# Kernel optimization log

Measured on AMD Instinct MI355X. Metric: run time of the kernel, lower is better.

Reference implementation:

```python
import jax, jax.numpy as jnp
import numpy as np

B, T, H, W = 2, 16, 16, 16
C_IN, C_ORIG, N_RES, KC, VC = 256, 3, 4, 16, 128
C_ATT = C_IN + C_ORIG          # 259, used for 1/sqrt(c) scale
C_PE = C_ATT + 3               # 262, conv input channels after pos-enc concat
NEG = jnp.float32(-1e30)


def setup_inputs() -> dict:
    key = jax.random.key(0)
    ks = jax.random.split(key, 12)
    f32 = jnp.float32

    def wt(k, shape, fan_in):
        return (jax.random.normal(k, shape, dtype=f32) / np.float32(np.sqrt(fan_in)))

    return {
        "x": jax.random.normal(ks[0], (B, C_IN, T, H, W), dtype=f32),
        "original_input": jax.random.normal(ks[1], (B, C_ORIG, T, H, W), dtype=f32),
        # residual blocks (stacked over N_RES): kernel-2 conv3d, padding 1
        "rb_w1": wt(ks[2], (N_RES, C_IN, C_IN, 2, 2, 2), C_IN * 8),
        "rb_b1": jnp.zeros((N_RES, C_IN), f32),
        "rb_w2": wt(ks[3], (N_RES, 2 * C_IN, C_IN, 2, 2, 2), C_IN * 8),
        "rb_b2": jnp.zeros((N_RES, 2 * C_IN), f32),
        # attention q/k/v 1x1 conv3d == per-pixel linear on 262 channels
        "q_w": wt(ks[4], (KC, C_PE), C_PE), "q_b": jnp.zeros((KC,), f32),
        "k_w": wt(ks[5], (KC, C_PE), C_PE), "k_b": jnp.zeros((KC,), f32),
        "v_w": wt(ks[6], (VC, C_PE), C_PE), "v_b": jnp.zeros((VC,), f32),
        # attention_conv (1x1), res_conv (1x1), out_conv (1x1)
        "attn_w": wt(ks[7], (C_IN, VC), VC), "attn_b": jnp.zeros((C_IN,), f32),
        "resc_w": wt(ks[8], (C_IN, C_IN), C_IN), "resc_b": jnp.zeros((C_IN,), f32),
        "out_w": wt(ks[9], (C_IN, C_IN), C_IN), "out_b": jnp.zeros((C_IN,), f32),
    }


def _conv3d(x, w, b, pad):
    y = jax.lax.conv_general_dilated(
        x, w, window_strides=(1, 1, 1), padding=[(pad, pad)] * 3,
        dimension_numbers=("NCDHW", "OIDHW", "NCDHW"))
    return y + b[None, :, None, None, None]


def _c1(x, w, b):  # 1x1x1 conv
    return jnp.einsum("bcthw,oc->bothw", x, w) + b[None, :, None, None, None]


def _pos_enc(b, t, h, w):
    zt = (-0.5 + jnp.arange(t, dtype=jnp.float32) / t)[None, None, :, None, None]
    zh = (-0.5 + jnp.arange(h, dtype=jnp.float32) / h)[None, None, None, :, None]
    zw = (-0.5 + jnp.arange(w, dtype=jnp.float32) / w)[None, None, None, None, :]
    shp = (b, 1, t, h, w)
    return jnp.concatenate([jnp.broadcast_to(zt, shp),
                            jnp.broadcast_to(zh, shp),
                            jnp.broadcast_to(zw, shp)], axis=1)


def _forward(x, original_input, rb_w1, rb_b1, rb_w2, rb_b2,
             q_w, q_b, k_w, k_b, v_w, v_b,
             attn_w, attn_b, resc_w, resc_b, out_w, out_b):
    b, _, t, h, w = x.shape
    elu = jax.nn.elu

    # --- residual blocks (attention=True variant: k=2 convs, pad=1, crop) ---
    res = x
    for i in range(N_RES):
        o = elu(_conv3d(elu(res), rb_w1[i], rb_b1[i], 1))[:, :, :t, :h, :w]
        o = _conv3d(o, rb_w2[i], rb_b2[i], 1)[:, :, :t, :h, :w]
        c2 = o.shape[1] // 2
        res = res + o[:, :c2] * jax.nn.sigmoid(o[:, c2:])  # gated (identity act)

    # --- attention block on concat(res, original_input) + pos-enc ---
    xa = jnp.concatenate([res, original_input], axis=1)          # (b,259,t,h,w)
    xa = jnp.concatenate([xa, _pos_enc(b, t, h, w)], axis=1)     # (b,262,t,h,w)
    seq = t * h * w
    xf = xa.reshape(b, C_PE, seq).transpose(0, 2, 1)             # (b,seq,262)
    q = xf @ q_w.T + q_b
    k = xf @ k_w.T + k_b
    v = xf @ v_w.T + v_b                                         # (b,seq,VC)

    scores = jnp.einsum("bqc,bkc->bqk", q, k) / np.float32(np.sqrt(C_ATT))
    mask = jnp.tril(jnp.ones((seq, seq), dtype=bool), k=-1)      # mask_center=True
    p = jax.nn.softmax(jnp.where(mask, scores, NEG), axis=-1)
    p = jnp.where(mask, p, 0.0)                                  # row 0 -> zeros
    att = jnp.einsum("bqk,bkc->bqc", p, v)                       # (b,seq,VC)
    att = att.transpose(0, 2, 1).reshape(b, VC, t, h, w)

    att = elu(_c1(elu(att), attn_w, attn_b))
    res = elu(_c1(elu(res), resc_w, resc_b))
    return elu(_c1(elu(res + att), out_w, out_b))


def reference(x, original_input, rb_w1, rb_b1, rb_w2, rb_b2,
              q_w, q_b, k_w, k_b, v_w, v_b,
              attn_w, attn_b, resc_w, resc_b, out_w, out_b):
    return _forward(x, original_input, rb_w1, rb_b1, rb_w2, rb_b2,
                    q_w, q_b, k_w, k_b, v_w, v_b,
                    attn_w, attn_b, resc_w, resc_b, out_w, out_b)
```

## Files before the change

### kernel.cpp

```cpp
#include <hip/hip_runtime.h>
#include <math.h>

#define SEQ 4096
#define CIN 256
#define PROWS 4913
#define PT 289
#define LROW 40
#define NROWS 170

typedef __attribute__((ext_vector_type(8))) short bf16x8;
typedef __attribute__((ext_vector_type(4))) float f32x4;

__device__ __forceinline__ float elu_f(float x) {
    return x > 0.0f ? x : (expf(x) - 1.0f);
}
__device__ __forceinline__ unsigned short f2b(float f) {
    unsigned int u = __float_as_uint(f);
    return (unsigned short)((u + 0x7FFFu + ((u >> 16) & 1u)) >> 16);
}

__global__ __launch_bounds__(256) void zero2_kernel(
    uint4* __restrict__ p1, uint4* __restrict__ p2, int n)
{
    int i = blockIdx.x * 256 + threadIdx.x;
    if (i < n) {
        p1[i] = (uint4){0, 0, 0, 0};
        p2[i] = (uint4){0, 0, 0, 0};
    }
}

__global__ __launch_bounds__(256) void prep_t(
    const float* __restrict__ x, unsigned short* __restrict__ elub)
{
    const int b = blockIdx.x >> 5;
    const int s0 = (blockIdx.x & 31) << 7;
    const int cg = blockIdx.y;
    const int tid = threadIdx.x;
    const int s = s0 + (tid & 127);
    const int c0 = cg * 32 + (tid >> 7) * 16;
    const int tt = s >> 8, hh = (s >> 4) & 15, ww = s & 15;
    const size_t prow = (size_t)b * PROWS + (tt + 1) * PT + (hh + 1) * 17 + (ww + 1);
    unsigned short ev[16];
#pragma unroll
    for (int cc = 0; cc < 16; ++cc) {
        float v = x[(((size_t)(b * 256 + c0 + cc)) << 12) + s];
        ev[cc] = f2b(elu_f(v));
    }
    unsigned short* ep = &elub[prow * 256 + c0];
    *(ushort4*)(ep)      = *(ushort4*)&ev[0];
    *(ushort4*)(ep + 4)  = *(ushort4*)&ev[4];
    *(ushort4*)(ep + 8)  = *(ushort4*)&ev[8];
    *(ushort4*)(ep + 12) = *(ushort4*)&ev[12];
}

__global__ __launch_bounds__(256) void wcvt_kernel(
    const float* __restrict__ w1, const float* __restrict__ w2,
    unsigned short* __restrict__ w1t, unsigned short* __restrict__ w2t)
{
    int idx = blockIdx.x * 256 + threadIdx.x;
    if (idx < 2097152) {
        int layer = idx >> 19;
        int rem = idx & 0x7FFFF;
        int frag = rem >> 9;
        int l = (rem >> 3) & 63;
        int e = rem & 7;
        int ks = frag >> 4, mt = frag & 15;
        int tap = ks >> 3, kc = ks & 7;
        int co = mt * 16 + (l & 15);
        int ci = kc * 32 + (l >> 4) * 8 + e;
        w1t[idx] = f2b(w1[(((size_t)(layer * 256 + co)) * 256 + ci) * 8 + tap]);
    }
    if (idx < 4194304) {
        int layer = idx >> 20;
        int rem = idx & 0xFFFFF;
        int frag = rem >> 9;
        int l = (rem >> 3) & 63;
        int e = rem & 7;
        int ks = frag >> 5, mt = frag & 31;
        int tap = ks >> 3, kc = ks & 7;
        int rp = mt * 16 + (l & 15);
        int grp = rp >> 5, sub = rp & 31;
        int co = (sub < 16) ? (grp * 16 + sub) : (256 + grp * 16 + (sub - 16));
        int ci = kc * 32 + (l >> 4) * 8 + e;
        w2t[idx] = f2b(w2[(((size_t)(layer * 512 + co)) * 256 + ci) * 8 + tap]);
    }
}

__global__ __launch_bounds__(256) void conv1_mfma(
    const unsigned short* __restrict__ inP,
    const unsigned short* __restrict__ wfrag,
    const float* __restrict__ bias,
    unsigned short* __restrict__ outP)
{
    __shared__ unsigned short sX[NROWS * LROW];

    const int bx = blockIdx.x;
    const int b = bx >> 6, ptile = bx & 63;
    const int t = ptile >> 2, h0 = (ptile & 3) << 2;
    const int mt0 = blockIdx.y << 2;
    const int tid = threadIdx.x;
    const int lane = tid & 63, wv = tid >> 6;
    const int lr = lane & 15, lg = lane >> 4;

    const unsigned short* inB = inP + (size_t)b * PROWS * 256;

    f32x4 acc[4];
#pragma unroll
    for (int mi = 0; mi < 4; ++mi) acc[mi] = (f32x4){0.f, 0.f, 0.f, 0.f};

    for (int kc = 0; kc < 8; ++kc) {
        const int ci0 = kc << 5;
        __syncthreads();
#pragma unroll
        for (int rnd = 0; rnd < 3; ++rnd) {
            int task = tid + (rnd << 8);
            int row = task >> 2, q = task & 3;
            if (row < NROWS) {
                int dt = row / 85, rem = row - dt * 85;
                int dh = rem / 17, dw = rem - dh * 17;
                int prow = (t + dt) * PT + (h0 + dh) * 17 + dw;
                *(bf16x8*)&sX[row * LROW + (q << 3)] =
                    *(const bf16x8*)(inB + (size_t)prow * 256 + ci0 + (q << 3));
            }
        }
        __syncthreads();
#pragma unroll
        for (int tap = 0; tap < 8; ++tap) {
            const unsigned short* wp = wfrag +
                ((size_t)((((tap << 3) + kc) << 4) + mt0) << 9) + (lane << 3);
            bf16x8 a0 = *(const bf16x8*)(wp);
            bf16x8 a1 = *(const bf16x8*)(wp + 512);
            bf16x8 a2 = *(const bf16x8*)(wp + 1024);
            bf16x8 a3 = *(const bf16x8*)(wp + 1536);
            const int rb = (tap >> 2) * 85 + (wv + ((tap >> 1) & 1)) * 17 + (tap & 1);
            bf16x8 xb = *(const bf16x8*)&sX[(rb + lr) * LROW + (lg << 3)];
            acc[0] = __builtin_amdgcn_mfma_f32_16x16x32_bf16(a0, xb, acc[0], 0, 0, 0);
            acc[1] = __builtin_amdgcn_mfma_f32_16x16x32_bf16(a1, xb, acc[1], 0, 0, 0);
            acc[2] = __builtin_amdgcn_mfma_f32_16x16x32_bf16(a2, xb, acc[2], 0, 0, 0);
            acc[3] = __builtin_amdgcn_mfma_f32_16x16x32_bf16(a3, xb, acc[3], 0, 0, 0);
        }
    }
    const size_t orow = (size_t)b * PROWS + (t + 1) * PT + (h0 + wv + 1) * 17 + (lr + 1);
#pragma unroll
    for (int mi = 0; mi < 4; ++mi) {
        const int cob = ((mt0 + mi) << 4) + (lg << 2);
        unsigned short v4[4];
#pragma unroll
        for (int r = 0; r < 4; ++r)
            v4[r] = f2b(elu_f(acc[mi][r] + bias[cob + r]));
        *(ushort4*)&outP[orow * 256 + cob] = *(ushort4*)v4;
    }
}

__global__ __launch_bounds__(256) void conv2_mfma(
    const unsigned short* __restrict__ inP,
    const unsigned short* __restrict__ wfrag,
    const float* __restrict__ bias,
    float* __restrict__ resf,
    unsigned short* __restrict__ elub)
{
    __shared__ unsigned short sX[NROWS * LROW];

    const int bx = blockIdx.x;
    const int b = bx >> 6, ptile = bx & 63;
    const int t = ptile >> 2, h0 = (ptile & 3) << 2;
    const int mt0 = blockIdx.y << 2;
    const int tid = threadIdx.x;
    const int lane = tid & 63, wv = tid >> 6;
    const int lr = lane & 15, lg = lane >> 4;

    const unsigned short* inB = inP + (size_t)b * PROWS * 256;

    f32x4 acc[4];
#pragma unroll
    for (int mi = 0; mi < 4; ++mi) acc[mi] = (f32x4){0.f, 0.f, 0.f, 0.f};

    for (int kc = 0; kc < 8; ++kc) {
        const int ci0 = kc << 5;
        __syncthreads();
#pragma unroll
        for (int rnd = 0; rnd < 3; ++rnd) {
            int task = tid + (rnd << 8);
            int row = task >> 2, q = task & 3;
            if (row < NROWS) {
                int dt = row / 85, rem = row - dt * 85;
                int dh = rem / 17, dw = rem - dh * 17;
                int prow = (t + dt) * PT + (h0 + dh) * 17 + dw;
                *(bf16x8*)&sX[row * LROW + (q << 3)] =
                    *(const bf16x8*)(inB + (size_t)prow * 256 + ci0 + (q << 3));
            }
        }
        __syncthreads();
#pragma unroll
        for (int tap = 0; tap < 8; ++tap) {
            const unsigned short* wp = wfrag +
                ((size_t)((((tap << 3) + kc) << 5) + mt0) << 9) + (lane << 3);
            bf16x8 a0 = *(const bf16x8*)(wp);
            bf16x8 a1 = *(const bf16x8*)(wp + 512);
            bf16x8 a2 = *(const bf16x8*)(wp + 1024);
            bf16x8 a3 = *(const bf16x8*)(wp + 1536);
            const int rb = (tap >> 2) * 85 + (wv + ((tap >> 1) & 1)) * 17 + (tap & 1);
            bf16x8 xb = *(const bf16x8*)&sX[(rb + lr) * LROW + (lg << 3)];
            acc[0] = __builtin_amdgcn_mfma_f32_16x16x32_bf16(a0, xb, acc[0], 0, 0, 0);
            acc[1] = __builtin_amdgcn_mfma_f32_16x16x32_bf16(a1, xb, acc[1], 0, 0, 0);
            acc[2] = __builtin_amdgcn_mfma_f32_16x16x32_bf16(a2, xb, acc[2], 0, 0, 0);
            acc[3] = __builtin_amdgcn_mfma_f32_16x16x32_bf16(a3, xb, acc[3], 0, 0, 0);
        }
    }
    const int s = (t << 8) + ((h0 + wv) << 4) + lr;
    const size_t prow = (size_t)b * PROWS + (t + 1) * PT + (h0 + wv + 1) * 17 + (lr + 1);
#pragma unroll
    for (int p = 0; p < 2; ++p) {
        const int chb = (((mt0 >> 1) + p) << 4) + (lg << 2);
        unsigned short e4[4];
#pragma unroll
        for (int r = 0; r < 4; ++r) {
            const int ch = chb + r;
            float av = acc[2 * p][r] + bias[ch];
            float gv = acc[2 * p + 1][r] + bias[ch + 256];
            float add = av / (1.0f + expf(-gv));
            size_t ridx = (((size_t)(b * 256 + ch)) << 12) + s;
            float rn = resf[ridx] + add;
            resf[ridx] = rn;
            e4[r] = f2b(elu_f(rn));
        }
        *(ushort4*)&elub[prow * 256 + chb] = *(ushort4*)e4;
    }
}

__global__ __launch_bounds__(256) void pack_kernel(
    const float* __restrict__ res, const float* __restrict__ orig,
    unsigned short* __restrict__ xq)
{
    const int b = blockIdx.x >> 5;
    const int s0 = (blockIdx.x & 31) << 7;
    const int cg = blockIdx.y;
    const int tid = threadIdx.x;
    const int s = s0 + (tid & 127);
    const int c0 = cg * 32 + (tid >> 7) * 16;

    unsigned short xv[16];
    if (cg < 8) {
#pragma unroll
        for (int cc = 0; cc < 16; ++cc) {
            int c = c0 + cc;
            float v = res[(size_t)((b * 256 + c) << 12) + s];
            xv[cc] = f2b(v);
        }
    } else if (cg == 8) {
#pragma unroll
        for (int cc = 0; cc < 16; ++cc) {
            int c = c0 + cc;
            float v;
            if (c < 259)      v = orig[(size_t)((b * 3 + (c - 256)) << 12) + s];
            else if (c == 259) v = -0.5f + (float)(s >> 8) * 0.0625f;
            else if (c == 260) v = -0.5f + (float)((s >> 4) & 15) * 0.0625f;
            else if (c == 261) v = -0.5f + (float)(s & 15) * 0.0625f;
            else               v = 0.0f;
            xv[cc] = f2b(v);
        }
    } else {
#pragma unroll
        for (int cc = 0; cc < 16; ++cc) xv[cc] = 0;
    }
    unsigned short* xp = &xq[((size_t)(b << 12) + s) * 320 + c0];
    *(ushort4*)(xp)      = *(ushort4*)&xv[0];
    *(ushort4*)(xp + 4)  = *(ushort4*)&xv[4];
    *(ushort4*)(xp + 8)  = *(ushort4*)&xv[8];
    *(ushort4*)(xp + 12) = *(ushort4*)&xv[12];
}

__global__ __launch_bounds__(256) void wcvt2_kernel(
    const float* __restrict__ qw, const float* __restrict__ kw,
    const float* __restrict__ vw, const float* __restrict__ aw,
    const float* __restrict__ rw, const float* __restrict__ ow,
    unsigned short* __restrict__ wqkv, unsigned short* __restrict__ awb,
    unsigned short* __restrict__ rwb, unsigned short* __restrict__ owb)
{
    int idx = blockIdx.x * 256 + threadIdx.x;
    if (idx < 61440) {
        int r = idx / 320, c = idx - r * 320;
        float v = 0.0f;
        if (c < 262) {
            if (r < 16)       v = qw[r * 262 + c];
            else if (r < 32)  v = kw[(r - 16) * 262 + c];
            else if (r < 160) v = vw[(r - 32) * 262 + c];
        }
        wqkv[idx] = f2b(v);
    } else if (idx < 61440 + 32768) {
        int j = idx - 61440; awb[j] = f2b(aw[j]);
    } else if (idx < 61440 + 32768 + 65536) {
        int j = idx - 61440 - 32768; rwb[j] = f2b(rw[j]);
    } else if (idx < 61440 + 32768 + 131072) {
        int j = idx - 61440 - 98304; owb[j] = f2b(ow[j]);
    }
}

__global__ __launch_bounds__(256) void qkv_gemm(
    const unsigned short* __restrict__ Wb, const unsigned short* __restrict__ Xt,
    const float* __restrict__ qb, const float* __restrict__ kb,
    const float* __restrict__ vb,
    unsigned short* __restrict__ qbt, unsigned short* __restrict__ kbt,
    unsigned short* __restrict__ vbt)
{
    const int b = blockIdx.x >> 5;
    const int s0 = (blockIdx.x & 31) << 7;
    const int co0 = blockIdx.y << 6;
    const int lane = threadIdx.x & 63, wv = threadIdx.x >> 6;
    const int lr = lane & 15, lg = lane >> 4;

    f32x4 acc[4][2];
#pragma unroll
    for (int mi = 0; mi < 4; ++mi)
#pragma unroll
        for (int ni = 0; ni < 2; ++ni) acc[mi][ni] = (f32x4){0.f, 0.f, 0.f, 0.f};

    const unsigned short* wp = Wb + (size_t)co0 * 320 + lg * 8;
    const unsigned short* xp = Xt + ((size_t)(b << 12) + s0 + wv * 32) * 320 + lg * 8;

#pragma unroll
    for (int kc = 0; kc < 10; ++kc) {
        int ko = kc * 32;
        bf16x8 a[4], x[2];
#pragma unroll
        for (int mi = 0; mi < 4; ++mi)
            a[mi] = *(const bf16x8*)(wp + (size_t)(mi * 16 + lr) * 320 + ko);
#pragma unroll
        for (int ni = 0; ni < 2; ++ni)
            x[ni] = *(const bf16x8*)(xp + (size_t)(ni * 16 + lr) * 320 + ko);
#pragma unroll
        for (int mi = 0; mi < 4; ++mi)
#pragma unroll
            for (int ni = 0; ni < 2; ++ni)
                acc[mi][ni] = __builtin_amdgcn_mfma_f32_16x16x32_bf16(
                    a[mi], x[ni], acc[mi][ni], 0, 0, 0);
    }
#pragma unroll
    for (int mi = 0; mi < 4; ++mi)
#pragma unroll
    for (int ni = 0; ni < 2; ++ni)
#pragma unroll
    for (int r = 0; r < 4; ++r) {
        int co = co0 + mi * 16 + lg * 4 + r;
        if (co >= 160) continue;
        int s = s0 + wv * 32 + ni * 16 + lr;
        float bias = (co < 16) ? qb[co] : ((co < 32) ? kb[co - 16] : vb[co - 32]);
        float v = acc[mi][ni][r] + bias;
        if (co < 16)      qbt[((size_t)(b << 12) + s) * 16 + co] = f2b(v);
        else if (co < 32) kbt[((size_t)(b << 12) + s) * 16 + (co - 16)] = f2b(v);
        else              vbt[((size_t)((b << 7) + (co - 32)) << 12) + s] = f2b(v);
    }
}

__global__ __launch_bounds__(256) void attn_part2(
    const unsigned short* __restrict__ qbt, const unsigned short* __restrict__ kbt,
    const unsigned short* __restrict__ vbt,
    float* __restrict__ pacc, float* __restrict__ pml)
{
    const int bx = blockIdx.x;
    const int b = bx >> 8;
    const int qt = (bx >> 2) & 63;
    const int seg = bx & 3;
    const int q0 = qt << 6;
    const int nch = (qt >> 1) + 1;
    const int c_lo = seg << 3;
    if (c_lo >= nch) return;
    const int c_hi = min(c_lo + 8, nch);

    __shared__ unsigned short sK[128 * 16];
    __shared__ unsigned short sP[4][16 * 136];

    const int tid = threadIdx.x;
    const int lane = tid & 63, wv = tid >> 6;
    const int lr = lane & 15, lg = lane >> 4;
    const int qa = q0 + wv * 16 + lr;
    const float scale = 1.0f / sqrtf(259.0f);

    bf16x8 qf = (bf16x8){0, 0, 0, 0, 0, 0, 0, 0};
    if (lg < 2)
        qf = *(const bf16x8*)(qbt + ((size_t)(b << 12) + qa) * 16 + lg * 8);

    f32x4 oacc[8];
#pragma unroll
    for (int vct = 0; vct < 8; ++vct) oacc[vct] = (f32x4){0.f, 0.f, 0.f, 0.f};
    float m = -1e30f, l = 0.0f;

    unsigned short* myP = &sP[wv][0];

    for (int kc = c_lo; kc < c_hi; ++kc) {
        const int kv0 = kc << 7;
        __syncthreads();
        *(bf16x8*)&sK[(tid >> 1) * 16 + (tid & 1) * 8] =
            *(const bf16x8*)(kbt + ((size_t)(b << 12) + kv0 + (tid >> 1)) * 16 + (tid & 1) * 8);
        __syncthreads();

        f32x4 sc[8];
#pragma unroll
        for (int kvt = 0; kvt < 8; ++kvt) {
            bf16x8 af = (bf16x8){0, 0, 0, 0, 0, 0, 0, 0};
            if (lg < 2)
                af = *(const bf16x8*)&sK[(kvt * 16 + lr) * 16 + lg * 8];
            sc[kvt] = __builtin_amdgcn_mfma_f32_16x16x32_bf16(
                af, qf, (f32x4){0.f, 0.f, 0.f, 0.f}, 0, 0, 0);
        }
        float mc = -1e30f;
#pragma unroll
        for (int kvt = 0; kvt < 8; ++kvt) {
#pragma unroll
            for (int r = 0; r < 4; ++r) {
                int kv = kv0 + kvt * 16 + lg * 4 + r;
                float s = (kv < qa) ? sc[kvt][r] * scale : -1e30f;
                sc[kvt][r] = s;
                mc = fmaxf(mc, s);
            }
        }
        mc = fmaxf(mc, __shfl_xor(mc, 16, 64));
        mc = fmaxf(mc, __shfl_xor(mc, 32, 64));
        float mn = fmaxf(m, mc);
        float fac = __expf(m - mn);
        float ls = 0.0f;
#pragma unroll
        for (int kvt = 0; kvt < 8; ++kvt) {
#pragma unroll
            for (int e = 0; e < 2; ++e) {
                float s0v = sc[kvt][2 * e];
                float s1v = sc[kvt][2 * e + 1];
                float p0 = (s0v <= -1e29f) ? 0.f : __expf(s0v - mn);
                float p1 = (s1v <= -1e29f) ? 0.f : __expf(s1v - mn);
                ls += p0 + p1;
                unsigned int pk = (unsigned int)f2b(p0) | ((unsigned int)f2b(p1) << 16);
                int kv = kvt * 16 + lg * 4 + 2 * e;
                *(unsigned int*)&myP[lr * 136 + kv] = pk;
            }
        }
        ls += __shfl_xor(ls, 16, 64);
        ls += __shfl_xor(ls, 32, 64);
        l = l * fac + ls;
        m = mn;
#pragma unroll
        for (int vct = 0; vct < 8; ++vct) {
            oacc[vct][0] *= fac; oacc[vct][1] *= fac;
            oacc[vct][2] *= fac; oacc[vct][3] *= fac;
        }
#pragma unroll
        for (int ks = 0; ks < 4; ++ks) {
            bf16x8 pf = *(const bf16x8*)&myP[lr * 136 + ks * 32 + lg * 8];
#pragma unroll
            for (int vct = 0; vct < 8; ++vct) {
                bf16x8 vf = *(const bf16x8*)(vbt +
                    ((size_t)((b << 7) + vct * 16 + lr) << 12) + kv0 + ks * 32 + lg * 8);
                oacc[vct] = __builtin_amdgcn_mfma_f32_16x16x32_bf16(
                    vf, pf, oacc[vct], 0, 0, 0);
            }
        }
    }

    const int a_ = qt >> 4;
    const int slot = b * 160 + 8 * a_ * (a_ + 1) + (qt & 15) * (a_ + 1) + seg;
    float* ap = pacc + (size_t)slot * 8192;
#pragma unroll
    for (int vct = 0; vct < 8; ++vct)
        *(f32x4*)&ap[(wv * 16 + lr) * 128 + vct * 16 + lg * 4] = oacc[vct];
    if (lg == 0) {
        pml[slot * 128 + (wv * 16 + lr) * 2]     = m;
        pml[slot * 128 + (wv * 16 + lr) * 2 + 1] = l;
    }
}

__global__ __launch_bounds__(256) void attn_combine2(
    const float* __restrict__ pacc, const float* __restrict__ pml,
    unsigned short* __restrict__ attEb)
{
    const int bx = blockIdx.x;
    const int b = bx >> 7;
    const int qt = (bx >> 1) & 63;
    const int half = bx & 1;
    const int a_ = qt >> 4;
    const int nseg_alloc = a_ + 1;
    const int nch = (qt >> 1) + 1;
    const int nseg = (nch + 7) >> 3;
    const int base = b * 160 + 8 * a_ * (a_ + 1) + (qt & 15) * nseg_alloc;
    const int tid = threadIdx.x;
    const int qq = (tid >> 3) + half * 32;
    const int vg = tid & 7;

    float mi_[4], li_[4];
    float m = -1e30f;
    for (int i = 0; i < nseg; ++i) {
        mi_[i] = pml[(base + i) * 128 + qq * 2];
        li_[i] = pml[(base + i) * 128 + qq * 2 + 1];
        m = fmaxf(m, mi_[i]);
    }
    float w[4];
    float l = 0.f;
    for (int i = 0; i < nseg; ++i) {
        float wi = (mi_[i] <= -1e29f) ? 0.f : __expf(mi_[i] - m);
        w[i] = wi;
        l += wi * li_[i];
    }
    float inv = (l > 0.f) ? 1.f / l : 0.f;
    int q = (qt << 6) + qq;
#pragma unroll
    for (int v4 = 0; v4 < 4; ++v4) {
        int vc = vg * 16 + v4 * 4;
        float o0 = 0.f, o1 = 0.f, o2 = 0.f, o3 = 0.f;
        for (int i = 0; i < nseg; ++i) {
            f32x4 a = *(const f32x4*)(pacc + (size_t)(base + i) * 8192 + qq * 128 + vc);
            o0 = fmaf(w[i], a[0], o0);
            o1 = fmaf(w[i], a[1], o1);
            o2 = fmaf(w[i], a[2], o2);
            o3 = fmaf(w[i], a[3], o3);
        }
        unsigned short r0 = f2b(elu_f(o0 * inv));
        unsigned short r1 = f2b(elu_f(o1 * inv));
        unsigned short r2 = f2b(elu_f(o2 * inv));
        unsigned short r3 = f2b(elu_f(o3 * inv));
        ushort4 pk = {r0, r1, r2, r3};
        *(ushort4*)&attEb[((size_t)(b << 12) + q) * 128 + vc] = pk;
    }
}

__global__ __launch_bounds__(256) void final_ab_gemm(
    const unsigned short* __restrict__ W1b, const unsigned short* __restrict__ W2b,
    const unsigned short* __restrict__ X1, const unsigned short* __restrict__ X2,
    const float* __restrict__ b1, const float* __restrict__ b2,
    unsigned short* __restrict__ sum2b)
{
    const int b = blockIdx.x >> 5;
    const int s0 = (blockIdx.x & 31) << 7;
    const int co0 = blockIdx.y << 6;
    const int lane = threadIdx.x & 63, wv = threadIdx.x >> 6;
    const int lr = lane & 15, lg = lane >> 4;

    f32x4 acc1[4][2], acc2[4][2];
#pragma unroll
    for (int mi = 0; mi < 4; ++mi)
#pragma unroll
        for (int ni = 0; ni < 2; ++ni) {
            acc1[mi][ni] = (f32x4){0.f, 0.f, 0.f, 0.f};
            acc2[mi][ni] = (f32x4){0.f, 0.f, 0.f, 0.f};
        }

    {
        const unsigned short* wp = W1b + (size_t)co0 * 128 + lg * 8;
        const unsigned short* xp = X1 + ((size_t)(b << 12) + s0 + wv * 32) * 128 + lg * 8;
#pragma unroll
        for (int kc = 0; kc < 4; ++kc) {
            int ko = kc * 32;
            bf16x8 a[4], x[2];
#pragma unroll
            for (int mi = 0; mi < 4; ++mi)
                a[mi] = *(const bf16x8*)(wp + (size_t)(mi * 16 + lr) * 128 + ko);
#pragma unroll
            for (int ni = 0; ni < 2; ++ni)
                x[ni] = *(const bf16x8*)(xp + (size_t)(ni * 16 + lr) * 128 + ko);
#pragma unroll
            for (int mi = 0; mi < 4; ++mi)
#pragma unroll
                for (int ni = 0; ni < 2; ++ni)
                    acc1[mi][ni] = __builtin_amdgcn_mfma_f32_16x16x32_bf16(
                        a[mi], x[ni], acc1[mi][ni], 0, 0, 0);
        }
    }
    {
        const unsigned short* wp = W2b + (size_t)co0 * 256 + lg * 8;
        const unsigned short* xp2[2];
#pragma unroll
        for (int ni = 0; ni < 2; ++ni) {
            int u = (s0 >> 4) + wv * 2 + ni;
            int tt = u >> 4, hh = u & 15;
            xp2[ni] = X2 + ((size_t)b * PROWS + (tt + 1) * PT + (hh + 1) * 17 + (lr + 1)) * 256 + lg * 8;
        }
#pragma unroll
        for (int kc = 0; kc < 8; ++kc) {
            int ko = kc * 32;
            bf16x8 a[4], x[2];
#pragma unroll
            for (int mi = 0; mi < 4; ++mi)
                a[mi] = *(const bf16x8*)(wp + (size_t)(mi * 16 + lr) * 256 + ko);
#pragma unroll
            for (int ni = 0; ni < 2; ++ni)
                x[ni] = *(const bf16x8*)(xp2[ni] + ko);
#pragma unroll
            for (int mi = 0; mi < 4; ++mi)
#pragma unroll
                for (int ni = 0; ni < 2; ++ni)
                    acc2[mi][ni] = __builtin_amdgcn_mfma_f32_16x16x32_bf16(
                        a[mi], x[ni], acc2[mi][ni], 0, 0, 0);
        }
    }
#pragma unroll
    for (int mi = 0; mi < 4; ++mi)
#pragma unroll
    for (int ni = 0; ni < 2; ++ni)
#pragma unroll
    for (int r = 0; r < 4; ++r) {
        int co = co0 + mi * 16 + lg * 4 + r;
        int s = s0 + wv * 32 + ni * 16 + lr;
        float v1 = elu_f(acc1[mi][ni][r] + b1[co]);
        float v2 = elu_f(acc2[mi][ni][r] + b2[co]);
        sum2b[((size_t)(b << 12) + s) * 256 + co] = f2b(elu_f(v1 + v2));
    }
}

__global__ __launch_bounds__(256) void final_c_gemm(
    const unsigned short* __restrict__ Wb, const unsigned short* __restrict__ Xt,
    const float* __restrict__ bias, float* __restrict__ out)
{
    const int b = blockIdx.x >> 5;
    const int s0 = (blockIdx.x & 31) << 7;
    const int co0 = blockIdx.y << 6;
    const int lane = threadIdx.x & 63, wv = threadIdx.x >> 6;
    const int lr = lane & 15, lg = lane >> 4;

    f32x4 acc[4][2];
#pragma unroll
    for (int mi = 0; mi < 4; ++mi)
#pragma unroll
        for (int ni = 0; ni < 2; ++ni) acc[mi][ni] = (f32x4){0.f, 0.f, 0.f, 0.f};

    const unsigned short* wp = Wb + (size_t)co0 * 256 + lg * 8;
    const unsigned short* xp = Xt + ((size_t)(b << 12) + s0 + wv * 32) * 256 + lg * 8;
#pragma unroll
    for (int kc = 0; kc < 8; ++kc) {
        int ko = kc * 32;
        bf16x8 a[4], x[2];
#pragma unroll
        for (int mi = 0; mi < 4; ++mi)
            a[mi] = *(const bf16x8*)(wp + (size_t)(mi * 16 + lr) * 256 + ko);
#pragma unroll
        for (int ni = 0; ni < 2; ++ni)
            x[ni] = *(const bf16x8*)(xp + (size_t)(ni * 16 + lr) * 256 + ko);
#pragma unroll
        for (int mi = 0; mi < 4; ++mi)
#pragma unroll
            for (int ni = 0; ni < 2; ++ni)
                acc[mi][ni] = __builtin_amdgcn_mfma_f32_16x16x32_bf16(
                    a[mi], x[ni], acc[mi][ni], 0, 0, 0);
    }
#pragma unroll
    for (int mi = 0; mi < 4; ++mi)
#pragma unroll
    for (int ni = 0; ni < 2; ++ni)
#pragma unroll
    for (int r = 0; r < 4; ++r) {
        int co = co0 + mi * 16 + lg * 4 + r;
        int s = s0 + wv * 32 + ni * 16 + lr;
        out[((size_t)(b * 256 + co) << 12) + s] = elu_f(acc[mi][ni][r] + bias[co]);
    }
}

extern "C" void kernel_launch(void* const* d_in, const int* in_sizes, int n_in,
                              void* d_out, int out_size, void* d_ws, size_t ws_size,
                              hipStream_t stream) {
    const float* x      = (const float*)d_in[0];
    const float* orig   = (const float*)d_in[1];
    const float* rb_w1  = (const float*)d_in[2];
    const float* rb_b1  = (const float*)d_in[3];
    const float* rb_w2  = (const float*)d_in[4];
    const float* rb_b2  = (const float*)d_in[5];
    const float* q_w    = (const float*)d_in[6];
    const float* q_b    = (const float*)d_in[7];
    const float* k_w    = (const float*)d_in[8];
    const float* k_b    = (const float*)d_in[9];
    const float* v_w    = (const float*)d_in[10];
    const float* v_b    = (const float*)d_in[11];
    const float* attn_w = (const float*)d_in[12];
    const float* attn_b = (const float*)d_in[13];
    const float* resc_w = (const float*)d_in[14];
    const float* resc_b = (const float*)d_in[15];
    const float* out_w  = (const float*)d_in[16];
    const float* out_b  = (const float*)d_in[17];
    float* out = (float*)d_out;

    char* base = (char*)d_ws;
    float*          res   = (float*)(base);
    unsigned short* elubP = (unsigned short*)(base + (8u << 20));
    unsigned short* o1P   = (unsigned short*)(base + (13u << 20));
    unsigned short* w1t   = (unsigned short*)(base + (18u << 20));
    unsigned short* w2t   = (unsigned short*)(base + (22u << 20));
    unsigned short* vbt   = o1P;
    unsigned short* attEb = (unsigned short*)(base + (15u << 20));
    unsigned short* sum2b = w1t;
    unsigned short* xqkvB = w2t;
    float*          pacc  = (float*)(base + (22u << 20));
    unsigned short* qbt   = (unsigned short*)(base + (32u << 20));
    unsigned short* kbt   = (unsigned short*)(base + (32u << 20) + 262144);
    unsigned short* wqkvB = (unsigned short*)(base + (32u << 20) + 524288);
    unsigned short* attnWb= (unsigned short*)(base + (32u << 20) + 655360);
    unsigned short* rescWb= (unsigned short*)(base + (32u << 20) + 720896);
    unsigned short* outWb = (unsigned short*)(base + (32u << 20) + 851968);
    float*          pml   = (float*)(base + (32u << 20) + 983040);

    const int nz = (2 * PROWS * 256 * 2) / 16;
    zero2_kernel<<<(nz + 255) / 256, 256, 0, stream>>>(
        (uint4*)elubP, (uint4*)o1P, nz);

    hipMemcpyAsync(res, x, (size_t)2097152 * sizeof(float),
                   hipMemcpyDeviceToDevice, stream);
    prep_t<<<dim3(64, 8), 256, 0, stream>>>(x, elubP);
    wcvt_kernel<<<16384, 256, 0, stream>>>(rb_w1, rb_w2, w1t, w2t);

    for (int i = 0; i < 4; ++i) {
        conv1_mfma<<<dim3(128, 4), 256, 0, stream>>>(
            elubP, w1t + (size_t)i * 524288, rb_b1 + i * 256, o1P);
        conv2_mfma<<<dim3(128, 8), 256, 0, stream>>>(
            o1P, w2t + (size_t)i * 1048576, rb_b2 + i * 512, res, elubP);
    }

    pack_kernel<<<dim3(64, 10), 256, 0, stream>>>(res, orig, xqkvB);
    wcvt2_kernel<<<880, 256, 0, stream>>>(q_w, k_w, v_w, attn_w, resc_w, out_w,
                                          wqkvB, attnWb, rescWb, outWb);

    qkv_gemm<<<dim3(64, 3), 256, 0, stream>>>(wqkvB, xqkvB, q_b, k_b, v_b,
                                              qbt, kbt, vbt);

    attn_part2<<<512, 256, 0, stream>>>(qbt, kbt, vbt, pacc, pml);
    attn_combine2<<<256, 256, 0, stream>>>(pacc, pml, attEb);

    final_ab_gemm<<<dim3(64, 4), 256, 0, stream>>>(
        attnWb, rescWb, attEb, elubP, attn_b, resc_b, sum2b);

    final_c_gemm<<<dim3(64, 4), 256, 0, stream>>>(outWb, sum2b, out_b, out);
}
```

Baseline: 424.0 us.

## Store V in MFMA fragment order and preload all K chunks into LDS

The QKV GEMM now writes V in a pre-swizzled layout that matches the MFMA operand fragment. Each lane in attention can then load its V fragment as one contiguous 16-byte read, replacing the earlier strided rows. The attention kernel also loads every K chunk for its segment into shared memory up front, which removes two barriers per iteration. The cost is a larger LDS footprint (32KB for K), which may lower occupancy, and scattered 2-byte stores in the GEMM epilogue.

```diff
diff --git a/kernel.cpp b/kernel.cpp
--- a/kernel.cpp
+++ b/kernel.cpp
@@ -301,7 +301,7 @@
     const float* __restrict__ qb, const float* __restrict__ kb,
     const float* __restrict__ vb,
     unsigned short* __restrict__ qbt, unsigned short* __restrict__ kbt,
-    unsigned short* __restrict__ vbt)
+    unsigned short* __restrict__ vfrag)
 {
     const int b = blockIdx.x >> 5;
     const int s0 = (blockIdx.x & 31) << 7;
@@ -348,13 +348,21 @@
         float v = acc[mi][ni][r] + bias;
         if (co < 16)      qbt[((size_t)(b << 12) + s) * 16 + co] = f2b(v);
         else if (co < 32) kbt[((size_t)(b << 12) + s) * 16 + (co - 16)] = f2b(v);
-        else              vbt[((size_t)((b << 7) + (co - 32)) << 12) + s] = f2b(v);
+        else {
+            int vc = co - 32;
+            int kvb = s >> 7, kvo = s & 127;
+            int ksv = kvo >> 5;
+            int lfrag = (((kvo >> 3) & 3) << 4) + (vc & 15);
+            size_t addr = ((((size_t)(b * 128 + kvb * 4 + ksv)) * 8 + (vc >> 4)) << 9)
+                          + (lfrag << 3) + (kvo & 7);
+            vfrag[addr] = f2b(v);
+        }
     }
 }
 
 __global__ __launch_bounds__(256) void attn_part2(
     const unsigned short* __restrict__ qbt, const unsigned short* __restrict__ kbt,
-    const unsigned short* __restrict__ vbt,
+    const unsigned short* __restrict__ vfrag,
     float* __restrict__ pacc, float* __restrict__ pml)
 {
     const int bx = blockIdx.x;
@@ -367,7 +375,7 @@
     if (c_lo >= nch) return;
     const int c_hi = min(c_lo + 8, nch);
 
-    __shared__ unsigned short sK[128 * 16];
+    __shared__ unsigned short sK[8 * 128 * 16];
     __shared__ unsigned short sP[4][16 * 136];
 
     const int tid = threadIdx.x;
@@ -380,6 +388,13 @@
     if (lg < 2)
         qf = *(const bf16x8*)(qbt + ((size_t)(b << 12) + qa) * 16 + lg * 8);
 
+    for (int kc = c_lo; kc < c_hi; ++kc) {
+        *(bf16x8*)&sK[((kc - c_lo) << 11) + (tid >> 1) * 16 + (tid & 1) * 8] =
+            *(const bf16x8*)(kbt + ((size_t)(b << 12) + (kc << 7) + (tid >> 1)) * 16
+                             + (tid & 1) * 8);
+    }
+    __syncthreads();
+
     f32x4 oacc[8];
 #pragma unroll
     for (int vct = 0; vct < 8; ++vct) oacc[vct] = (f32x4){0.f, 0.f, 0.f, 0.f};
@@ -388,18 +403,15 @@
     unsigned short* myP = &sP[wv][0];
 
     for (int kc = c_lo; kc < c_hi; ++kc) {
+        const int kci = kc - c_lo;
         const int kv0 = kc << 7;
-        __syncthreads();
-        *(bf16x8*)&sK[(tid >> 1) * 16 + (tid & 1) * 8] =
-            *(const bf16x8*)(kbt + ((size_t)(b << 12) + kv0 + (tid >> 1)) * 16 + (tid & 1) * 8);
-        __syncthreads();
 
         f32x4 sc[8];
 #pragma unroll
         for (int kvt = 0; kvt < 8; ++kvt) {
             bf16x8 af = (bf16x8){0, 0, 0, 0, 0, 0, 0, 0};
             if (lg < 2)
-                af = *(const bf16x8*)&sK[(kvt * 16 + lr) * 16 + lg * 8];
+                af = *(const bf16x8*)&sK[(kci << 11) + (kvt * 16 + lr) * 16 + lg * 8];
             sc[kvt] = __builtin_amdgcn_mfma_f32_16x16x32_bf16(
                 af, qf, (f32x4){0.f, 0.f, 0.f, 0.f}, 0, 0, 0);
         }
@@ -442,13 +454,14 @@
             oacc[vct][0] *= fac; oacc[vct][1] *= fac;
             oacc[vct][2] *= fac; oacc[vct][3] *= fac;
         }
+        const unsigned short* vchunk = vfrag +
+            ((size_t)(b * 128 + (kv0 >> 5)) << 12) + (lane << 3);
 #pragma unroll
         for (int ks = 0; ks < 4; ++ks) {
             bf16x8 pf = *(const bf16x8*)&myP[lr * 136 + ks * 32 + lg * 8];
 #pragma unroll
             for (int vct = 0; vct < 8; ++vct) {
-                bf16x8 vf = *(const bf16x8*)(vbt +
-                    ((size_t)((b << 7) + vct * 16 + lr) << 12) + kv0 + ks * 32 + lg * 8);
+                bf16x8 vf = *(const bf16x8*)(vchunk + ((size_t)(ks * 8 + vct) << 9));
                 oacc[vct] = __builtin_amdgcn_mfma_f32_16x16x32_bf16(
                     vf, pf, oacc[vct], 0, 0, 0);
             }
@@ -679,7 +692,7 @@
     unsigned short* o1P   = (unsigned short*)(base + (13u << 20));
     unsigned short* w1t   = (unsigned short*)(base + (18u << 20));
     unsigned short* w2t   = (unsigned short*)(base + (22u << 20));
-    unsigned short* vbt   = o1P;
+    unsigned short* vfrag = o1P;
     unsigned short* attEb = (unsigned short*)(base + (15u << 20));
     unsigned short* sum2b = w1t;
     unsigned short* xqkvB = w2t;
@@ -713,9 +726,9 @@
                                           wqkvB, attnWb, rescWb, outWb);
 
     qkv_gemm<<<dim3(64, 3), 256, 0, stream>>>(wqkvB, xqkvB, q_b, k_b, v_b,
-                                              qbt, kbt, vbt);
-
-    attn_part2<<<512, 256, 0, stream>>>(qbt, kbt, vbt, pacc, pml);
+                                              qbt, kbt, vfrag);
+
+    attn_part2<<<512, 256, 0, stream>>>(qbt, kbt, vfrag, pacc, pml);
     attn_combine2<<<256, 256, 0, stream>>>(pacc, pml, attEb);
 
     final_ab_gemm<<<dim3(64, 4), 256, 0, stream>>>(
```

After: 429.4 us. No clear change (+1.3%).

## Pre-swizzle GEMM weights into MFMA fragment order and stage activations in LDS

Applied to the files above, without the earlier changes.

Weight conversion now writes the q/k/v, attention, residual and output 1x1 weights in MFMA fragment-major order, so each lane loads its A operand with one contiguous 16-byte read. The three small GEMM kernels also copy 128-row activation tiles into padded shared memory with coalesced loads before the MFMA reads, replacing strided per-lane global loads. In exchange each k-step adds two block barriers and drops full unrolling, and there is no double buffering, so loads and MFMAs may serialize.

```diff
diff --git a/kernel.cpp b/kernel.cpp
--- a/kernel.cpp
+++ b/kernel.cpp
@@ -7,6 +7,7 @@
 #define PT 289
 #define LROW 40
 #define NROWS 170
+#define GROW 36
 
 typedef __attribute__((ext_vector_type(8))) short bf16x8;
 typedef __attribute__((ext_vector_type(4))) float f32x4;
@@ -279,7 +280,10 @@
 {
     int idx = blockIdx.x * 256 + threadIdx.x;
     if (idx < 61440) {
-        int r = idx / 320, c = idx - r * 320;
+        int frag = idx >> 9, l = (idx >> 3) & 63, e = idx & 7;
+        int kc = frag / 12, mt = frag - kc * 12;
+        int r = mt * 16 + (l & 15);
+        int c = kc * 32 + ((l >> 4) << 3) + e;
         float v = 0.0f;
         if (c < 262) {
             if (r < 16)       v = qw[r * 262 + c];
@@ -287,26 +291,44 @@
             else if (r < 160) v = vw[(r - 32) * 262 + c];
         }
         wqkv[idx] = f2b(v);
-    } else if (idx < 61440 + 32768) {
-        int j = idx - 61440; awb[j] = f2b(aw[j]);
-    } else if (idx < 61440 + 32768 + 65536) {
-        int j = idx - 61440 - 32768; rwb[j] = f2b(rw[j]);
-    } else if (idx < 61440 + 32768 + 131072) {
-        int j = idx - 61440 - 98304; owb[j] = f2b(ow[j]);
+    } else if (idx < 94208) {
+        int j = idx - 61440;
+        int frag = j >> 9, l = (j >> 3) & 63, e = j & 7;
+        int kc = frag >> 4, mt = frag & 15;
+        int r = mt * 16 + (l & 15);
+        int c = kc * 32 + ((l >> 4) << 3) + e;
+        awb[j] = f2b(aw[r * 128 + c]);
+    } else if (idx < 159744) {
+        int j = idx - 94208;
+        int frag = j >> 9, l = (j >> 3) & 63, e = j & 7;
+        int kc = frag >> 4, mt = frag & 15;
+        int r = mt * 16 + (l & 15);
+        int c = kc * 32 + ((l >> 4) << 3) + e;
+        rwb[j] = f2b(rw[r * 256 + c]);
+    } else if (idx < 225280) {
+        int j = idx - 159744;
+        int frag = j >> 9, l = (j >> 3) & 63, e = j & 7;
+        int kc = frag >> 4, mt = frag & 15;
+        int r = mt * 16 + (l & 15);
+        int c = kc * 32 + ((l >> 4) << 3) + e;
+        owb[j] = f2b(ow[r * 256 + c]);
     }
 }
 
 __global__ __launch_bounds__(256) void qkv_gemm(
-    const unsigned short* __restrict__ Wb, const unsigned short* __restrict__ Xt,
+    const unsigned short* __restrict__ Wf, const unsigned short* __restrict__ Xt,
     const float* __restrict__ qb, const float* __restrict__ kb,
     const float* __restrict__ vb,
     unsigned short* __restrict__ qbt, unsigned short* __restrict__ kbt,
     unsigned short* __restrict__ vbt)
 {
+    __shared__ unsigned short sX[128 * GROW];
+
     const int b = blockIdx.x >> 5;
     const int s0 = (blockIdx.x & 31) << 7;
-    const int co0 = blockIdx.y << 6;
-    const int lane = threadIdx.x & 63, wv = threadIdx.x >> 6;
+    const int mt0 = blockIdx.y << 2;
+    const int tid = threadIdx.x;
+    const int lane = tid & 63, wv = tid >> 6;
     const int lr = lane & 15, lg = lane >> 4;
 
     f32x4 acc[4][2];
@@ -315,26 +337,34 @@
 #pragma unroll
         for (int ni = 0; ni < 2; ++ni) acc[mi][ni] = (f32x4){0.f, 0.f, 0.f, 0.f};
 
-    const unsigned short* wp = Wb + (size_t)co0 * 320 + lg * 8;
-    const unsigned short* xp = Xt + ((size_t)(b << 12) + s0 + wv * 32) * 320 + lg * 8;
-
-#pragma unroll
     for (int kc = 0; kc < 10; ++kc) {
-        int ko = kc * 32;
-        bf16x8 a[4], x[2];
-#pragma unroll
-        for (int mi = 0; mi < 4; ++mi)
-            a[mi] = *(const bf16x8*)(wp + (size_t)(mi * 16 + lr) * 320 + ko);
-#pragma unroll
-        for (int ni = 0; ni < 2; ++ni)
-            x[ni] = *(const bf16x8*)(xp + (size_t)(ni * 16 + lr) * 320 + ko);
-#pragma unroll
-        for (int mi = 0; mi < 4; ++mi)
-#pragma unroll
-            for (int ni = 0; ni < 2; ++ni)
-                acc[mi][ni] = __builtin_amdgcn_mfma_f32_16x16x32_bf16(
-                    a[mi], x[ni], acc[mi][ni], 0, 0, 0);
-    }
+        __syncthreads();
+#pragma unroll
+        for (int rnd = 0; rnd < 2; ++rnd) {
+            int task = tid + (rnd << 8);
+            int row = task >> 2, q = task & 3;
+            *(bf16x8*)&sX[row * GROW + (q << 3)] =
+                *(const bf16x8*)(Xt + ((size_t)(b << 12) + s0 + row) * 320
+                                 + kc * 32 + (q << 3));
+        }
+        __syncthreads();
+        const unsigned short* wp = Wf + ((size_t)(kc * 12 + mt0) << 9) + (lane << 3);
+        bf16x8 a0 = *(const bf16x8*)(wp);
+        bf16x8 a1 = *(const bf16x8*)(wp + 512);
+        bf16x8 a2 = *(const bf16x8*)(wp + 1024);
+        bf16x8 a3 = *(const bf16x8*)(wp + 1536);
+        bf16x8 x0 = *(const bf16x8*)&sX[(wv * 32 + lr) * GROW + (lg << 3)];
+        bf16x8 x1 = *(const bf16x8*)&sX[(wv * 32 + 16 + lr) * GROW + (lg << 3)];
+        acc[0][0] = __builtin_amdgcn_mfma_f32_16x16x32_bf16(a0, x0, acc[0][0], 0, 0, 0);
+        acc[0][1] = __builtin_amdgcn_mfma_f32_16x16x32_bf16(a0, x1, acc[0][1], 0, 0, 0);
+        acc[1][0] = __builtin_amdgcn_mfma_f32_16x16x32_bf16(a1, x0, acc[1][0], 0, 0, 0);
+        acc[1][1] = __builtin_amdgcn_mfma_f32_16x16x32_bf16(a1, x1, acc[1][1], 0, 0, 0);
+        acc[2][0] = __builtin_amdgcn_mfma_f32_16x16x32_bf16(a2, x0, acc[2][0], 0, 0, 0);
+        acc[2][1] = __builtin_amdgcn_mfma_f32_16x16x32_bf16(a2, x1, acc[2][1], 0, 0, 0);
+        acc[3][0] = __builtin_amdgcn_mfma_f32_16x16x32_bf16(a3, x0, acc[3][0], 0, 0, 0);
+        acc[3][1] = __builtin_amdgcn_mfma_f32_16x16x32_bf16(a3, x1, acc[3][1], 0, 0, 0);
+    }
+    const int co0 = mt0 << 4;
 #pragma unroll
     for (int mi = 0; mi < 4; ++mi)
 #pragma unroll
@@ -521,15 +551,18 @@
 }
 
 __global__ __launch_bounds__(256) void final_ab_gemm(
-    const unsigned short* __restrict__ W1b, const unsigned short* __restrict__ W2b,
+    const unsigned short* __restrict__ W1f, const unsigned short* __restrict__ W2f,
     const unsigned short* __restrict__ X1, const unsigned short* __restrict__ X2,
     const float* __restrict__ b1, const float* __restrict__ b2,
     unsigned short* __restrict__ sum2b)
 {
+    __shared__ unsigned short sX[128 * GROW];
+
     const int b = blockIdx.x >> 5;
     const int s0 = (blockIdx.x & 31) << 7;
-    const int co0 = blockIdx.y << 6;
-    const int lane = threadIdx.x & 63, wv = threadIdx.x >> 6;
+    const int mt0 = blockIdx.y << 2;
+    const int tid = threadIdx.x;
+    const int lane = tid & 63, wv = tid >> 6;
     const int lr = lane & 15, lg = lane >> 4;
 
     f32x4 acc1[4][2], acc2[4][2];
@@ -541,54 +574,63 @@
             acc2[mi][ni] = (f32x4){0.f, 0.f, 0.f, 0.f};
         }
 
-    {
-        const unsigned short* wp = W1b + (size_t)co0 * 128 + lg * 8;
-        const unsigned short* xp = X1 + ((size_t)(b << 12) + s0 + wv * 32) * 128 + lg * 8;
-#pragma unroll
-        for (int kc = 0; kc < 4; ++kc) {
-            int ko = kc * 32;
-            bf16x8 a[4], x[2];
-#pragma unroll
-            for (int mi = 0; mi < 4; ++mi)
-                a[mi] = *(const bf16x8*)(wp + (size_t)(mi * 16 + lr) * 128 + ko);
-#pragma unroll
-            for (int ni = 0; ni < 2; ++ni)
-                x[ni] = *(const bf16x8*)(xp + (size_t)(ni * 16 + lr) * 128 + ko);
-#pragma unroll
-            for (int mi = 0; mi < 4; ++mi)
-#pragma unroll
-                for (int ni = 0; ni < 2; ++ni)
-                    acc1[mi][ni] = __builtin_amdgcn_mfma_f32_16x16x32_bf16(
-                        a[mi], x[ni], acc1[mi][ni], 0, 0, 0);
-        }
-    }
-    {
-        const unsigned short* wp = W2b + (size_t)co0 * 256 + lg * 8;
-        const unsigned short* xp2[2];
-#pragma unroll
-        for (int ni = 0; ni < 2; ++ni) {
-            int u = (s0 >> 4) + wv * 2 + ni;
-            int tt = u >> 4, hh = u & 15;
-            xp2[ni] = X2 + ((size_t)b * PROWS + (tt + 1) * PT + (hh + 1) * 17 + (lr + 1)) * 256 + lg * 8;
-        }
-#pragma unroll
-        for (int kc = 0; kc < 8; ++kc) {
-            int ko = kc * 32;
-            bf16x8 a[4], x[2];
-#pragma unroll
-            for (int mi = 0; mi < 4; ++mi)
-                a[mi] = *(const bf16x8*)(wp + (size_t)(mi * 16 + lr) * 256 + ko);
-#pragma unroll
-            for (int ni = 0; ni < 2; ++ni)
-                x[ni] = *(const bf16x8*)(xp2[ni] + ko);
-#pragma unroll
-            for (int mi = 0; mi < 4; ++mi)
-#pragma unroll
-                for (int ni = 0; ni < 2; ++ni)
-                    acc2[mi][ni] = __builtin_amdgcn_mfma_f32_16x16x32_bf16(
-                        a[mi], x[ni], acc2[mi][ni], 0, 0, 0);
-        }
-    }
+    for (int kc = 0; kc < 4; ++kc) {
+        __syncthreads();
+#pragma unroll
+        for (int rnd = 0; rnd < 2; ++rnd) {
+            int task = tid + (rnd << 8);
+            int row = task >> 2, q = task & 3;
+            *(bf16x8*)&sX[row * GROW + (q << 3)] =
+                *(const bf16x8*)(X1 + ((size_t)(b << 12) + s0 + row) * 128
+                                 + kc * 32 + (q << 3));
+        }
+        __syncthreads();
+        const unsigned short* wp = W1f + ((size_t)((kc << 4) + mt0) << 9) + (lane << 3);
+        bf16x8 a0 = *(const bf16x8*)(wp);
+        bf16x8 a1 = *(const bf16x8*)(wp + 512);
+        bf16x8 a2 = *(const bf16x8*)(wp + 1024);
+        bf16x8 a3 = *(const bf16x8*)(wp + 1536);
+        bf16x8 x0 = *(const bf16x8*)&sX[(wv * 32 + lr) * GROW + (lg << 3)];
+        bf16x8 x1 = *(const bf16x8*)&sX[(wv * 32 + 16 + lr) * GROW + (lg << 3)];
+        acc1[0][0] = __builtin_amdgcn_mfma_f32_16x16x32_bf16(a0, x0, acc1[0][0], 0, 0, 0);
+        acc1[0][1] = __builtin_amdgcn_mfma_f32_16x16x32_bf16(a0, x1, acc1[0][1], 0, 0, 0);
+        acc1[1][0] = __builtin_amdgcn_mfma_f32_16x16x32_bf16(a1, x0, acc1[1][0], 0, 0, 0);
+        acc1[1][1] = __builtin_amdgcn_mfma_f32_16x16x32_bf16(a1, x1, acc1[1][1], 0, 0, 0);
+        acc1[2][0] = __builtin_amdgcn_mfma_f32_16x16x32_bf16(a2, x0, acc1[2][0], 0, 0, 0);
+        acc1[2][1] = __builtin_amdgcn_mfma_f32_16x16x32_bf16(a2, x1, acc1[2][1], 0, 0, 0);
+        acc1[3][0] = __builtin_amdgcn_mfma_f32_16x16x32_bf16(a3, x0, acc1[3][0], 0, 0, 0);
+        acc1[3][1] = __builtin_amdgcn_mfma_f32_16x16x32_bf16(a3, x1, acc1[3][1], 0, 0, 0);
+    }
+    for (int kc = 0; kc < 8; ++kc) {
+        __syncthreads();
+#pragma unroll
+        for (int rnd = 0; rnd < 2; ++rnd) {
+            int task = tid + (rnd << 8);
+            int row = task >> 2, q = task & 3;
+            int s = s0 + row;
+            int tt = s >> 8, hh = (s >> 4) & 15, ww = s & 15;
+            size_t prow = (size_t)b * PROWS + (tt + 1) * PT + (hh + 1) * 17 + (ww + 1);
+            *(bf16x8*)&sX[row * GROW + (q << 3)] =
+                *(const bf16x8*)(X2 + prow * 256 + kc * 32 + (q << 3));
+        }
+        __syncthreads();
+        const unsigned short* wp = W2f + ((size_t)((kc << 4) + mt0) << 9) + (lane << 3);
+        bf16x8 a0 = *(const bf16x8*)(wp);
+        bf16x8 a1 = *(const bf16x8*)(wp + 512);
+        bf16x8 a2 = *(const bf16x8*)(wp + 1024);
+        bf16x8 a3 = *(const bf16x8*)(wp + 1536);
+        bf16x8 x0 = *(const bf16x8*)&sX[(wv * 32 + lr) * GROW + (lg << 3)];
+        bf16x8 x1 = *(const bf16x8*)&sX[(wv * 32 + 16 + lr) * GROW + (lg << 3)];
+        acc2[0][0] = __builtin_amdgcn_mfma_f32_16x16x32_bf16(a0, x0, acc2[0][0], 0, 0, 0);
+        acc2[0][1] = __builtin_amdgcn_mfma_f32_16x16x32_bf16(a0, x1, acc2[0][1], 0, 0, 0);
+        acc2[1][0] = __builtin_amdgcn_mfma_f32_16x16x32_bf16(a1, x0, acc2[1][0], 0, 0, 0);
+        acc2[1][1] = __builtin_amdgcn_mfma_f32_16x16x32_bf16(a1, x1, acc2[1][1], 0, 0, 0);
+        acc2[2][0] = __builtin_amdgcn_mfma_f32_16x16x32_bf16(a2, x0, acc2[2][0], 0, 0, 0);
+        acc2[2][1] = __builtin_amdgcn_mfma_f32_16x16x32_bf16(a2, x1, acc2[2][1], 0, 0, 0);
+        acc2[3][0] = __builtin_amdgcn_mfma_f32_16x16x32_bf16(a3, x0, acc2[3][0], 0, 0, 0);
+        acc2[3][1] = __builtin_amdgcn_mfma_f32_16x16x32_bf16(a3, x1, acc2[3][1], 0, 0, 0);
+    }
+    const int co0 = mt0 << 4;
 #pragma unroll
     for (int mi = 0; mi < 4; ++mi)
 #pragma unroll
@@ -604,13 +646,16 @@
 }
 
 __global__ __launch_bounds__(256) void final_c_gemm(
-    const unsigned short* __restrict__ Wb, const unsigned short* __restrict__ Xt,
+    const unsigned short* __restrict__ Wf, const unsigned short* __restrict__ Xt,
     const float* __restrict__ bias, float* __restrict__ out)
 {
+    __shared__ unsigned short sX[128 * GROW];
+
     const int b = blockIdx.x >> 5;
     const int s0 = (blockIdx.x & 31) << 7;
-    const int co0 = blockIdx.y << 6;
-    const int lane = threadIdx.x & 63, wv = threadIdx.x >> 6;
+    const int mt0 = blockIdx.y << 2;
+    const int tid = threadIdx.x;
+    const int lane = tid & 63, wv = tid >> 6;
     const int lr = lane & 15, lg = lane >> 4;
 
     f32x4 acc[4][2];
@@ -619,25 +664,34 @@
 #pragma unroll
         for (int ni = 0; ni < 2; ++ni) acc[mi][ni] = (f32x4){0.f, 0.f, 0.f, 0.f};
 
-    const unsigned short* wp = Wb + (size_t)co0 * 256 + lg * 8;
-    const unsigned short* xp = Xt + ((size_t)(b << 12) + s0 + wv * 32) * 256 + lg * 8;
-#pragma unroll
     for (int kc = 0; kc < 8; ++kc) {
-        int ko = kc * 32;
-        bf16x8 a[4], x[2];
-#pragma unroll
-        for (int mi = 0; mi < 4; ++mi)
-            a[mi] = *(const bf16x8*)(wp + (size_t)(mi * 16 + lr) * 256 + ko);
-#pragma unroll
-        for (int ni = 0; ni < 2; ++ni)
-            x[ni] = *(const bf16x8*)(xp + (size_t)(ni * 16 + lr) * 256 + ko);
-#pragma unroll
-        for (int mi = 0; mi < 4; ++mi)
-#pragma unroll
-            for (int ni = 0; ni < 2; ++ni)
-                acc[mi][ni] = __builtin_amdgcn_mfma_f32_16x16x32_bf16(
-                    a[mi], x[ni], acc[mi][ni], 0, 0, 0);
-    }
+        __syncthreads();
+#pragma unroll
+        for (int rnd = 0; rnd < 2; ++rnd) {
+            int task = tid + (rnd << 8);
+            int row = task >> 2, q = task & 3;
+            *(bf16x8*)&sX[row * GROW + (q << 3)] =
+                *(const bf16x8*)(Xt + ((size_t)(b << 12) + s0 + row) * 256
+                                 + kc * 32 + (q << 3));
+        }
+        __syncthreads();
+        const unsigned short* wp = Wf + ((size_t)((kc << 4) + mt0) << 9) + (lane << 3);
+        bf16x8 a0 = *(const bf16x8*)(wp);
+        bf16x8 a1 = *(const bf16x8*)(wp + 512);
+        bf16x8 a2 = *(const bf16x8*)(wp + 1024);
+        bf16x8 a3 = *(const bf16x8*)(wp + 1536);
+        bf16x8 x0 = *(const bf16x8*)&sX[(wv * 32 + lr) * GROW + (lg << 3)];
+        bf16x8 x1 = *(const bf16x8*)&sX[(wv * 32 + 16 + lr) * GROW + (lg << 3)];
+        acc[0][0] = __builtin_amdgcn_mfma_f32_16x16x32_bf16(a0, x0, acc[0][0], 0, 0, 0);
+        acc[0][1] = __builtin_amdgcn_mfma_f32_16x16x32_bf16(a0, x1, acc[0][1], 0, 0, 0);
+        acc[1][0] = __builtin_amdgcn_mfma_f32_16x16x32_bf16(a1, x0, acc[1][0], 0, 0, 0);
+        acc[1][1] = __builtin_amdgcn_mfma_f32_16x16x32_bf16(a1, x1, acc[1][1], 0, 0, 0);
+        acc[2][0] = __builtin_amdgcn_mfma_f32_16x16x32_bf16(a2, x0, acc[2][0], 0, 0, 0);
+        acc[2][1] = __builtin_amdgcn_mfma_f32_16x16x32_bf16(a2, x1, acc[2][1], 0, 0, 0);
+        acc[3][0] = __builtin_amdgcn_mfma_f32_16x16x32_bf16(a3, x0, acc[3][0], 0, 0, 0);
+        acc[3][1] = __builtin_amdgcn_mfma_f32_16x16x32_bf16(a3, x1, acc[3][1], 0, 0, 0);
+    }
+    const int co0 = mt0 << 4;
 #pragma unroll
     for (int mi = 0; mi < 4; ++mi)
 #pragma unroll
```

Result: no change. 420.6 us (median of 3 runs) (-0.8%).
